# Performance work log

Measured on AMD Instinct MI355X. Metric: run time of the kernel, lower is better.

## Reference

```python
import jax, jax.numpy as jnp
import numpy as np

FILTER_LENGTH = 32
STEP_SIZE = 0.1
EPS = 1e-08


def setup_inputs() -> dict:
    key = jax.random.key(0)
    k1, k2 = jax.random.split(key)
    B, T, F = 32, 2000, 513
    X_hat_mag = jax.random.uniform(k1, (B, T, F), dtype=jnp.float32)
    Y_mag = jax.random.uniform(k2, (B, T, F), dtype=jnp.float32)
    W_prev = jnp.zeros((B, FILTER_LENGTH, F), dtype=jnp.float32)
    return {"X_hat_mag": X_hat_mag, "Y_mag": Y_mag, "W_prev": W_prev}


def reference(X_hat_mag, Y_mag, W_prev):
    B, T, F = Y_mag.shape
    L = FILTER_LENGTH
    # Zero-pad L-1 frames at the front so window k is Xp[:, k:k+L, :],
    # matching the torch F.pad(..., (0,0,pad_len,0)) behavior for k < L.
    Xp = jnp.pad(X_hat_mag, ((0, 0), (L - 1, 0), (0, 0)))
    yT = jnp.transpose(Y_mag, (1, 0, 2))  # [T, B, F] for scan xs

    def step(W, inp):
        k, y = inp  # y: [B, F]
        Xw = jax.lax.dynamic_slice_in_dim(Xp, k, L, axis=1)  # [B, L, F]
        y_hat = jnp.sum(W * Xw, axis=1)                      # [B, F]
        e = y - y_hat                                        # [B, F]
        norm = jnp.sum(Xw * Xw, axis=1) + EPS                # [B, F]
        W = W + STEP_SIZE * (e / norm)[:, None, :] * Xw      # [B, L, F]
        return W, e

    W_final, E = jax.lax.scan(step, W_prev, (jnp.arange(T), yT))
    E_hat_mag = jnp.transpose(E, (1, 0, 2))  # [B, T, F]
    return E_hat_mag, W_final
```

## Files before the change

kernel.cpp:

```cpp
#include <hip/hip_runtime.h>


#define LF   32
#define TT   2000
#define FF   513
#define BB   32
#define STEPSZ 0.1f
#define EPSV   1e-8f
#define NP   16

__device__ __forceinline__ float dpp_swap1(float v) {
    return __int_as_float(
        __builtin_amdgcn_mov_dpp(__float_as_int(v), 0xB1, 0xF, 0xF, true));
}

__global__ __launch_bounds__(64, 1)
void nlms_kernel(const float* __restrict__ X, const float* __restrict__ Y,
                 const float* __restrict__ Wp, float* __restrict__ E,
                 float* __restrict__ Wout) {
    const int lane = threadIdx.x;
    const int half = lane & 1;
    const int prob = blockIdx.x * 32 + (lane >> 1);
    const int b = prob / FF;
    const int f = prob - b * FF;

    const float* Xc = X + (size_t)b * TT * FF + f;
    const float* Yc = Y + (size_t)b * TT * FF + f;
    float*       Ec = E + (size_t)b * TT * FF + f;
    const int colW = b * (LF * FF) + (16 * half) * FF + f;

    float W[16];
#pragma unroll
    for (int i = 0; i < 16; ++i) W[i] = Wp[colW + i * FF];

    float w[16];
#pragma unroll
    for (int i = 0; i < 16; ++i) w[i] = 0.0f;

    float xn[NP], yn[NP];
#pragma unroll
    for (int i = 0; i < NP; ++i) {
        xn[i] = Xc[i * FF];
        yn[i] = Yc[i * FF];
    }

    float s = 0.0f;

#pragma unroll 1
    for (int kk = 0; kk < TT; kk += NP) {
#pragma unroll
        for (int j = 0; j < NP; ++j) {
            const int k = kk + j;
            const float x_new = xn[j];
            const float y     = yn[j];

            int kp = k + NP; if (kp > TT - 1) kp = TT - 1;
            xn[j] = Xc[kp * FF];
            yn[j] = Yc[kp * FF];

            const float out = w[j];
            const float sh  = dpp_swap1(out);
            const float inc = half ? x_new
                                   : sh;
            w[j] = inc;

            s = fmaf(inc, inc, s);
            s = fmaf(-out, out, s);

            float a0 = 0.f, a1 = 0.f, a2 = 0.f, a3 = 0.f;
#pragma unroll
            for (int i = 0; i < 16; i += 4) {
                a0 = fmaf(W[i + 0], w[(j + 1 + i + 0) & 15], a0);
                a1 = fmaf(W[i + 1], w[(j + 1 + i + 1) & 15], a1);
                a2 = fmaf(W[i + 2], w[(j + 1 + i + 2) & 15], a2);
                a3 = fmaf(W[i + 3], w[(j + 1 + i + 3) & 15], a3);
            }
            const float part = (a0 + a1) + (a2 + a3);

            const float yh  = part + dpp_swap1(part);
            const float nrm = s + dpp_swap1(s);

            const float e = y - yh;
            const float d = nrm + EPSV;
            float r = __builtin_amdgcn_rcpf(d);
            r = r * fmaf(-d, r, 2.0f);
            const float c = (STEPSZ * e) * r;

#pragma unroll
            for (int i = 0; i < 16; ++i)
                W[i] = fmaf(c, w[(j + 1 + i) & 15], W[i]);

            if (half == 0) Ec[k * FF] = e;
        }
    }

#pragma unroll
    for (int i = 0; i < 16; ++i) Wout[colW + i * FF] = W[i];
}

extern "C" void kernel_launch(void* const* d_in, const int* in_sizes, int n_in,
                              void* d_out, int out_size, void* d_ws, size_t ws_size,
                              hipStream_t stream) {
    const float* X  = (const float*)d_in[0];
    const float* Y  = (const float*)d_in[1];
    const float* Wp = (const float*)d_in[2];
    float* E    = (float*)d_out;
    float* Wout = E + (size_t)BB * TT * FF;

    nlms_kernel<<<dim3(513), dim3(64), 0, stream>>>(X, Y, Wp, E, Wout);
}
```

Measured before the change: 582.6 us.

## Stage X/Y tiles through double-buffered LDS with direct global-to-LDS loads

Replaces the per-lane register prefetch of X and Y, where both lanes of each pair loaded the same value, with asynchronous global_load_lds transfers. Each lane loads one distinct element, and tiles of 16 timesteps go into double-buffered LDS, two tiles ahead. Each tile is read from LDS into registers before the serial NLMS recurrence runs. This halves the global load instructions and frees the prefetch registers. In exchange it relies on hand-written vmcnt/lgkmcnt waits whose counts must match the store and load interleaving.

```diff
diff --git a/kernel.cpp b/kernel.cpp
--- a/kernel.cpp
+++ b/kernel.cpp
@@ -7,26 +7,40 @@
 #define BB   32
 #define STEPSZ 0.1f
 #define EPSV   1e-8f
-#define NP   16
+#define NT   16
+#define NTILES (TT / NT)
 
 __device__ __forceinline__ float dpp_swap1(float v) {
     return __int_as_float(
         __builtin_amdgcn_mov_dpp(__float_as_int(v), 0xB1, 0xF, 0xF, true));
 }
 
+__device__ __forceinline__ void gload_lds(const float* g, float* l) {
+    __builtin_amdgcn_global_load_lds(
+        (const __attribute__((address_space(1))) void*)g,
+        (__attribute__((address_space(3))) void*)l, 4, 0, 0);
+}
+
 __global__ __launch_bounds__(64, 1)
 void nlms_kernel(const float* __restrict__ X, const float* __restrict__ Y,
                  const float* __restrict__ Wp, float* __restrict__ E,
                  float* __restrict__ Wout) {
+    __shared__ float xb[2][NT][32];
+    __shared__ float yb[2][NT][32];
+
     const int lane = threadIdx.x;
     const int half = lane & 1;
     const int prob = blockIdx.x * 32 + (lane >> 1);
     const int b = prob / FF;
     const int f = prob - b * FF;
 
-    const float* Xc = X + (size_t)b * TT * FF + f;
-    const float* Yc = Y + (size_t)b * TT * FF + f;
-    float*       Ec = E + (size_t)b * TT * FF + f;
+    const int ps = blockIdx.x * 32 + (lane & 31);
+    const int bs = ps / FF;
+    const int fs = ps - bs * FF;
+    const float* Xs = X + (size_t)bs * TT * FF + (size_t)(lane >> 5) * FF + fs;
+    const float* Ys = Y + (size_t)bs * TT * FF + (size_t)(lane >> 5) * FF + fs;
+
+    float*    Ec   = E + (size_t)b * TT * FF + f;
     const int colW = b * (LF * FF) + (16 * half) * FF + f;
 
     float W[16];
@@ -37,26 +51,42 @@
 #pragma unroll
     for (int i = 0; i < 16; ++i) w[i] = 0.0f;
 
-    float xn[NP], yn[NP];
-#pragma unroll
-    for (int i = 0; i < NP; ++i) {
-        xn[i] = Xc[i * FF];
-        yn[i] = Yc[i * FF];
-    }
-
     float s = 0.0f;
 
+#pragma unroll
+    for (int q = 0; q < NT / 2; ++q)
+        gload_lds(Xs + (size_t)(2 * q) * FF, &xb[0][2 * q][0]);
+#pragma unroll
+    for (int q = 0; q < NT / 2; ++q)
+        gload_lds(Ys + (size_t)(2 * q) * FF, &yb[0][2 * q][0]);
+#pragma unroll
+    for (int q = 0; q < NT / 2; ++q)
+        gload_lds(Xs + (size_t)(NT + 2 * q) * FF, &xb[1][2 * q][0]);
+#pragma unroll
+    for (int q = 0; q < NT / 2; ++q)
+        gload_lds(Ys + (size_t)(NT + 2 * q) * FF, &yb[1][2 * q][0]);
+
 #pragma unroll 1
-    for (int kk = 0; kk < TT; kk += NP) {
+    for (int tt = 0; tt < NTILES; ++tt) {
+        if (tt == 0 || tt == NTILES - 1)
+            asm volatile("s_waitcnt vmcnt(16)" ::: "memory");
+        else
+            asm volatile("s_waitcnt vmcnt(32)" ::: "memory");
+
+        const int buf = tt & 1;
+        const int p   = lane >> 1;
+
+        float xs[NT], ys[NT];
 #pragma unroll
-        for (int j = 0; j < NP; ++j) {
-            const int k = kk + j;
-            const float x_new = xn[j];
-            const float y     = yn[j];
+        for (int i = 0; i < NT; ++i) {
+            xs[i] = xb[buf][i][p];
+            ys[i] = yb[buf][i][p];
+        }
 
-            int kp = k + NP; if (kp > TT - 1) kp = TT - 1;
-            xn[j] = Xc[kp * FF];
-            yn[j] = Yc[kp * FF];
+#pragma unroll
+        for (int j = 0; j < NT; ++j) {
+            const float x_new = xs[j];
+            const float y     = ys[j];
 
             const float out = w[j];
             const float sh  = dpp_swap1(out);
@@ -90,7 +120,18 @@
             for (int i = 0; i < 16; ++i)
                 W[i] = fmaf(c, w[(j + 1 + i) & 15], W[i]);
 
-            if (half == 0) Ec[k * FF] = e;
+            if (half == 0) Ec[(tt * NT + j) * FF] = e;
+        }
+
+        if (tt + 2 < NTILES) {
+            asm volatile("s_waitcnt lgkmcnt(0)" ::: "memory");
+            const size_t t0 = (size_t)(tt + 2) * NT;
+#pragma unroll
+            for (int q = 0; q < NT / 2; ++q)
+                gload_lds(Xs + (t0 + 2 * q) * FF, &xb[buf][2 * q][0]);
+#pragma unroll
+            for (int q = 0; q < NT / 2; ++q)
+                gload_lds(Ys + (t0 + 2 * q) * FF, &yb[buf][2 * q][0]);
         }
     }
 
```

New measurement: 582.9 us. About the same (+0.1%).
